# Performance work log

Measured on AMD Instinct MI355X. Metric: run time of the kernel, lower is better.

The kernel has to match this reference:

```python
import jax, jax.numpy as jnp
import numpy as np

N_NODES = 100000
N_EDGES = 1200000
D_IN = 64
D_HID = 64


def setup_inputs() -> dict:
    key = jax.random.key(0)
    ks = jax.random.split(key, 8)
    s = 1.0 / np.sqrt(D_IN)
    return {
        "x": jax.random.normal(ks[0], (N_NODES, D_IN), dtype=jnp.float32),
        "edge_index": jax.random.randint(ks[1], (2, N_EDGES), 0, N_NODES, dtype=jnp.int64),
        "W1_rel": jax.random.normal(ks[2], (D_IN, D_HID), dtype=jnp.float32) * s,
        "W1_root": jax.random.normal(ks[3], (D_IN, D_HID), dtype=jnp.float32) * s,
        "b1": jnp.zeros((D_HID,), dtype=jnp.float32),
        "W2_rel": jax.random.normal(ks[4], (D_HID, D_HID), dtype=jnp.float32) * s,
        "W2_root": jax.random.normal(ks[5], (D_HID, D_HID), dtype=jnp.float32) * s,
        "b2": jnp.zeros((D_HID,), dtype=jnp.float32),
        "Wc": jax.random.normal(ks[6], (D_HID, 2), dtype=jnp.float32) * s,
        "bc": jnp.zeros((2,), dtype=jnp.float32),
    }


def graph_conv(x, src, dst, W_rel, W_root, b):
    # sum_{j in N(i)} x_j  (scatter-add of src features onto dst), then linear
    aggr = jax.ops.segment_sum(x[src], dst, num_segments=x.shape[0])
    return aggr @ W_rel + x @ W_root + b


def reference(x, edge_index, W1_rel, W1_root, b1, W2_rel, W2_root, b2, Wc, bc):
    src, dst = edge_index[0], edge_index[1]
    h = jax.nn.relu(graph_conv(x, src, dst, W1_rel, W1_root, b1))
    h = jax.nn.relu(graph_conv(h, src, dst, W2_rel, W2_root, b2))
    return h.mean(axis=0) @ Wc + bc  # [2]
```

## Files before the change

### kernel.cpp

```cpp
#include <hip/hip_runtime.h>

#define D 64
#define ROWTILE 32
#define XPAD 68

__global__ void detect_kernel(const void* __restrict__ e, int* __restrict__ flag) {
    if (threadIdx.x == 0 && blockIdx.x == 0) {
        const int* p = (const int*)e;
        int is64 = 1;
        for (int i = 1; i < 64; i += 2) {
            if (p[i] != 0) { is64 = 0; break; }
        }
        *flag = is64;
    }
}

__device__ __forceinline__ void load_edge(const void* __restrict__ eidx, int is64,
                                          int e, int nE, int& src, int& dst) {
    if (is64) {
        const long long* p = (const long long*)eidx;
        src = (int)p[e];
        dst = (int)p[nE + e];
    } else {
        const int* p = (const int*)eidx;
        src = p[e];
        dst = p[nE + e];
    }
}

__global__ __launch_bounds__(256) void hist_kernel(
    const void* __restrict__ eidx, const int* __restrict__ flag,
    int* __restrict__ count, int nE)
{
    const int is64 = *flag;
    int e = blockIdx.x * 256 + threadIdx.x;
    if (e >= nE) return;
    int src, dst;
    load_edge(eidx, is64, e, nE, src, dst);
    atomicAdd(&count[dst], 1);
}

__global__ __launch_bounds__(256) void scan1_kernel(
    const int* __restrict__ count, int* __restrict__ offs,
    int* __restrict__ bsum, int N)
{
    __shared__ int tmp[256];
    const int tid = threadIdx.x;
    const int i = blockIdx.x * 256 + tid;
    int v = (i < N) ? count[i] : 0;
    tmp[tid] = v;
    __syncthreads();
#pragma unroll
    for (int off = 1; off < 256; off <<= 1) {
        int t = (tid >= off) ? tmp[tid - off] : 0;
        __syncthreads();
        tmp[tid] += t;
        __syncthreads();
    }
    int incl = tmp[tid];
    if (i < N) offs[i] = incl - v;
    if (tid == 255) bsum[blockIdx.x] = incl;
}

__global__ __launch_bounds__(1024) void scan2_kernel(int* __restrict__ bsum, int nblk)
{
    __shared__ int tmp[1024];
    const int tid = threadIdx.x;
    int v = (tid < nblk) ? bsum[tid] : 0;
    tmp[tid] = v;
    __syncthreads();
#pragma unroll
    for (int off = 1; off < 1024; off <<= 1) {
        int t = (tid >= off) ? tmp[tid - off] : 0;
        __syncthreads();
        tmp[tid] += t;
        __syncthreads();
    }
    if (tid < nblk) bsum[tid] = tmp[tid] - v;
}

__global__ __launch_bounds__(256) void scan3_kernel(
    int* __restrict__ offs, const int* __restrict__ bsum,
    int* __restrict__ cursor, int N, int E)
{
    const int i = blockIdx.x * 256 + threadIdx.x;
    if (i < N) {
        int v = offs[i] + bsum[blockIdx.x];
        offs[i] = v;
        cursor[i] = v;
    }
    if (i == 0) offs[N] = E;
}

__global__ __launch_bounds__(256) void scatterpos_kernel(
    const void* __restrict__ eidx, const int* __restrict__ flag,
    int* __restrict__ cursor, int* __restrict__ ssrc, int nE)
{
    const int is64 = *flag;
    int e = blockIdx.x * 256 + threadIdx.x;
    if (e >= nE) return;
    int src, dst;
    load_edge(eidx, is64, e, nE, src, dst);
    int pos = atomicAdd(&cursor[dst], 1);
    ssrc[pos] = src;
}

__global__ __launch_bounds__(256) void gather_aggr_kernel(
    const float* __restrict__ feat, const int* __restrict__ ssrc,
    const int* __restrict__ offs, float* __restrict__ aggr, int N)
{
    const int g = threadIdx.x >> 4;
    const int c = threadIdx.x & 15;
    const int n = blockIdx.x * 16 + g;
    if (n >= N) return;
    const int e0 = offs[n], e1 = offs[n + 1];
    float4 acc = make_float4(0.f, 0.f, 0.f, 0.f);
    for (int e = e0; e < e1; ++e) {
        int s = ssrc[e];
        float4 v = *(const float4*)(feat + (long long)s * D + c * 4);
        acc.x += v.x; acc.y += v.y; acc.z += v.z; acc.w += v.w;
    }
    *(float4*)(aggr + (long long)n * D + c * 4) = acc;
}

template <bool WRITE_OUT, bool WRITE_PART>
__global__ __launch_bounds__(256, 3) void linear_relu_kernel(
    const float* __restrict__ in, const float* __restrict__ aggr,
    const float* __restrict__ Wrel, const float* __restrict__ Wroot,
    const float* __restrict__ bias,
    float* __restrict__ out, float* __restrict__ acc_out, int N)
{
    __shared__ float xs[ROWTILE][XPAD];
    __shared__ float gs[ROWTILE][XPAD];
    __shared__ float pb[2][16][XPAD];
    __shared__ float red[4][D];

    const int tid  = threadIdx.x;
    const int lane = tid & 63;
    const int wid  = tid >> 6;
    const int pair = wid >> 1;
    const int role = wid & 1;

    float wv[D];
    {
        const float* W = role ? Wrel : Wroot;
#pragma unroll
        for (int k = 0; k < D; ++k) wv[k] = W[k * D + lane];
    }
    const float bv = bias[lane];

    float csum = 0.f;
    const int ntiles = (N + ROWTILE - 1) / ROWTILE;
    for (int tile = blockIdx.x; tile < ntiles; tile += gridDim.x) {
        const long long rowbase = (long long)tile * ROWTILE;
        __syncthreads();
#pragma unroll
        for (int it = 0; it < 2; ++it) {
            const int i = it * 256 + tid;
            const int r = i >> 4;
            const int c = i & 15;
            long long row = rowbase + r;
            if (row >= N) row = N - 1;
            const long long off = row * D + c * 4;
            *(float4*)&xs[r][c * 4] = *(const float4*)(in + off);
            *(float4*)&gs[r][c * 4] = *(const float4*)(aggr + off);
        }
        __syncthreads();
        float part[16];
#pragma unroll
        for (int g = 0; g < 4; ++g) {
            const int r0 = pair * 16 + g * 4;
            float a0 = 0.f, a1 = 0.f, a2 = 0.f, a3 = 0.f;
            const float (*src)[XPAD] = role ? gs : xs;
#pragma unroll
            for (int k4 = 0; k4 < D / 4; ++k4) {
                float4 f0 = *(const float4*)&src[r0 + 0][k4 * 4];
                float4 f1 = *(const float4*)&src[r0 + 1][k4 * 4];
                float4 f2 = *(const float4*)&src[r0 + 2][k4 * 4];
                float4 f3 = *(const float4*)&src[r0 + 3][k4 * 4];
                const float w0 = wv[4 * k4 + 0], w1 = wv[4 * k4 + 1];
                const float w2 = wv[4 * k4 + 2], w3 = wv[4 * k4 + 3];
                a0 = fmaf(f0.x, w0, a0); a0 = fmaf(f0.y, w1, a0);
                a0 = fmaf(f0.z, w2, a0); a0 = fmaf(f0.w, w3, a0);
                a1 = fmaf(f1.x, w0, a1); a1 = fmaf(f1.y, w1, a1);
                a1 = fmaf(f1.z, w2, a1); a1 = fmaf(f1.w, w3, a1);
                a2 = fmaf(f2.x, w0, a2); a2 = fmaf(f2.y, w1, a2);
                a2 = fmaf(f2.z, w2, a2); a2 = fmaf(f2.w, w3, a2);
                a3 = fmaf(f3.x, w0, a3); a3 = fmaf(f3.y, w1, a3);
                a3 = fmaf(f3.z, w2, a3); a3 = fmaf(f3.w, w3, a3);
            }
            part[g * 4 + 0] = a0; part[g * 4 + 1] = a1;
            part[g * 4 + 2] = a2; part[g * 4 + 3] = a3;
        }
        if (role == 1) {
#pragma unroll
            for (int r = 0; r < 16; ++r) pb[pair][r][lane] = part[r];
        }
        __syncthreads();
        if (role == 0) {
#pragma unroll
            for (int r = 0; r < 16; ++r) {
                const long long grow = rowbase + pair * 16 + r;
                const float o = fmaxf(part[r] + pb[pair][r][lane] + bv, 0.f);
                if (grow < N) {
                    if (WRITE_OUT) out[grow * D + lane] = o;
                    if (WRITE_PART) csum += o;
                }
            }
        }
    }

    if (WRITE_PART) {
        __syncthreads();
        red[wid][lane] = csum;
        __syncthreads();
        if (tid < D) {
            float s = red[0][tid] + red[1][tid] + red[2][tid] + red[3][tid];
            unsafeAtomicAdd(&acc_out[tid], s);
        }
    }
}

__global__ void final_kernel(const float* __restrict__ acc,
                             const float* __restrict__ Wc, const float* __restrict__ bc,
                             float* __restrict__ out, float invN)
{
    const int lane = threadIdx.x;
    float m  = acc[lane] * invN;
    float o0 = m * Wc[lane * 2 + 0];
    float o1 = m * Wc[lane * 2 + 1];
#pragma unroll
    for (int off = 32; off > 0; off >>= 1) {
        o0 += __shfl_down(o0, off);
        o1 += __shfl_down(o1, off);
    }
    if (lane == 0) {
        out[0] = o0 + bc[0];
        out[1] = o1 + bc[1];
    }
}

extern "C" void kernel_launch(void* const* d_in, const int* in_sizes, int n_in,
                              void* d_out, int out_size, void* d_ws, size_t ws_size,
                              hipStream_t stream)
{
    const float* x       = (const float*)d_in[0];
    const void*  eidx    = d_in[1];
    const float* W1_rel  = (const float*)d_in[2];
    const float* W1_root = (const float*)d_in[3];
    const float* b1      = (const float*)d_in[4];
    const float* W2_rel  = (const float*)d_in[5];
    const float* W2_root = (const float*)d_in[6];
    const float* b2      = (const float*)d_in[7];
    const float* Wc      = (const float*)d_in[8];
    const float* bc      = (const float*)d_in[9];
    float* out = (float*)d_out;

    const int N = in_sizes[0] / D;
    const int E = in_sizes[1] / 2;

    auto align256 = [](size_t v) { return (v + 255) & ~(size_t)255; };

    char* p = (char*)d_ws;
    const size_t featBytes = align256((size_t)N * D * sizeof(float));
    float* aggr   = (float*)p; p += featBytes;
    float* h1     = (float*)p; p += featBytes;
    float* acc    = (float*)p; p += align256((size_t)D * sizeof(float));
    int*   count  = (int*)p;   p += align256((size_t)N * sizeof(int));
    int*   cursor = (int*)p;   p += align256((size_t)N * sizeof(int));
    int*   offs   = (int*)p;   p += align256(((size_t)N + 1) * sizeof(int));
    int*   bsum   = (int*)p;   p += align256((size_t)1024 * sizeof(int));
    int*   ssrc   = (int*)p;   p += align256((size_t)E * sizeof(int));
    int*   flag   = (int*)p;

    const int eblocks = (E + 255) / 256;
    const int nblk    = (N + 255) / 256;

    detect_kernel<<<1, 64, 0, stream>>>(eidx, flag);
    hipMemsetAsync(count, 0, (size_t)N * sizeof(int), stream);
    hipMemsetAsync(acc, 0, (size_t)D * sizeof(float), stream);
    hist_kernel<<<eblocks, 256, 0, stream>>>(eidx, flag, count, E);
    scan1_kernel<<<nblk, 256, 0, stream>>>(count, offs, bsum, N);
    scan2_kernel<<<1, 1024, 0, stream>>>(bsum, nblk);
    scan3_kernel<<<nblk, 256, 0, stream>>>(offs, bsum, cursor, N, E);
    scatterpos_kernel<<<eblocks, 256, 0, stream>>>(eidx, flag, cursor, ssrc, E);

    const int ablocks = (N + 15) / 16;

    gather_aggr_kernel<<<ablocks, 256, 0, stream>>>(x, ssrc, offs, aggr, N);
    linear_relu_kernel<true, false><<<1024, 256, 0, stream>>>(
        x, aggr, W1_rel, W1_root, b1, h1, nullptr, N);

    gather_aggr_kernel<<<ablocks, 256, 0, stream>>>(h1, ssrc, offs, aggr, N);
    linear_relu_kernel<false, true><<<1024, 256, 0, stream>>>(
        h1, aggr, W2_rel, W2_root, b2, nullptr, acc, N);

    final_kernel<<<1, 64, 0, stream>>>(acc, Wc, bc, out, 1.0f / (float)N);
}
```

Before: 438.5 us.

## Replace per-edge global atomic CSR scatter with two-level bucketed scatter

Replaces the per-edge global atomicAdd cursor scatter with two passes. The first sorts each 4096-edge chunk in shared memory into 256-node buckets and writes them with one global atomic per bucket. The second builds the CSR per bucket using LDS atomics. The goal is to remove heavy global atomic contention and scattered writes across 100k cursors, at the cost of an extra 8-byte-per-edge intermediate buffer and an extra kernel. It also unrolls the gather loop.

New measurement: 362.2 us. -17.4%, faster.

```diff
diff --git a/kernel.cpp b/kernel.cpp
--- a/kernel.cpp
+++ b/kernel.cpp
@@ -3,6 +3,8 @@
 #define D 64
 #define ROWTILE 32
 #define XPAD 68
+#define CHUNK 4096
+#define NBMAX 512
 
 __global__ void detect_kernel(const void* __restrict__ e, int* __restrict__ flag) {
     if (threadIdx.x == 0 && blockIdx.x == 0) {
@@ -80,29 +82,102 @@
 }
 
 __global__ __launch_bounds__(256) void scan3_kernel(
-    int* __restrict__ offs, const int* __restrict__ bsum,
-    int* __restrict__ cursor, int N, int E)
+    int* __restrict__ offs, const int* __restrict__ bsum, int N, int E)
 {
     const int i = blockIdx.x * 256 + threadIdx.x;
-    if (i < N) {
-        int v = offs[i] + bsum[blockIdx.x];
-        offs[i] = v;
-        cursor[i] = v;
-    }
+    if (i < N) offs[i] += bsum[blockIdx.x];
     if (i == 0) offs[N] = E;
 }
 
-__global__ __launch_bounds__(256) void scatterpos_kernel(
+__global__ __launch_bounds__(256) void bucket_scatter_kernel(
     const void* __restrict__ eidx, const int* __restrict__ flag,
-    int* __restrict__ cursor, int* __restrict__ ssrc, int nE)
-{
+    const int* __restrict__ offs, int* __restrict__ gbcur,
+    uint2* __restrict__ ebuk, int nE, int N, int nbk)
+{
+    __shared__ int bcnt[NBMAX];
+    __shared__ int boffs[NBMAX];
+    __shared__ int brun[NBMAX];
+    __shared__ int gbase[NBMAX];
+    __shared__ int bstart[NBMAX];
+    __shared__ int ps[256];
+    __shared__ uint2 staged[CHUNK];
+
     const int is64 = *flag;
-    int e = blockIdx.x * 256 + threadIdx.x;
-    if (e >= nE) return;
-    int src, dst;
-    load_edge(eidx, is64, e, nE, src, dst);
-    int pos = atomicAdd(&cursor[dst], 1);
-    ssrc[pos] = src;
+    const int tid = threadIdx.x;
+    const int e0 = blockIdx.x * CHUNK;
+    const int ec = min(CHUNK, nE - e0);
+
+    for (int i = tid; i < NBMAX; i += 256) { bcnt[i] = 0; brun[i] = 0; }
+    for (int i = tid; i < nbk; i += 256) bstart[i] = offs[i << 8];
+    __syncthreads();
+
+#pragma unroll
+    for (int j = 0; j < CHUNK / 256; ++j) {
+        const int i = j * 256 + tid;
+        if (i < ec) {
+            int s, d;
+            load_edge(eidx, is64, e0 + i, nE, s, d);
+            atomicAdd(&bcnt[d >> 8], 1);
+        }
+    }
+    __syncthreads();
+
+    const int c0 = bcnt[2 * tid], c1 = bcnt[2 * tid + 1];
+    ps[tid] = c0 + c1;
+    __syncthreads();
+#pragma unroll
+    for (int off = 1; off < 256; off <<= 1) {
+        int t = (tid >= off) ? ps[tid - off] : 0;
+        __syncthreads();
+        ps[tid] += t;
+        __syncthreads();
+    }
+    const int pexcl = ps[tid] - (c0 + c1);
+    boffs[2 * tid]     = pexcl;
+    boffs[2 * tid + 1] = pexcl + c0;
+    if (c0 > 0) gbase[2 * tid]     = atomicAdd(&gbcur[2 * tid], c0);
+    if (c1 > 0) gbase[2 * tid + 1] = atomicAdd(&gbcur[2 * tid + 1], c1);
+    __syncthreads();
+
+#pragma unroll
+    for (int j = 0; j < CHUNK / 256; ++j) {
+        const int i = j * 256 + tid;
+        if (i < ec) {
+            int s, d;
+            load_edge(eidx, is64, e0 + i, nE, s, d);
+            const int b = d >> 8;
+            const int p = boffs[b] + atomicAdd(&brun[b], 1);
+            staged[p] = make_uint2((unsigned)s, (unsigned)d);
+        }
+    }
+    __syncthreads();
+
+    for (int i = tid; i < ec; i += 256) {
+        const uint2 ent = staged[i];
+        const int b = (int)(ent.y >> 8);
+        const int pos = bstart[b] + gbase[b] + (i - boffs[b]);
+        ebuk[pos] = ent;
+    }
+}
+
+__global__ __launch_bounds__(256) void bucket_csr_kernel(
+    const uint2* __restrict__ ebuk, const int* __restrict__ offs,
+    int* __restrict__ ssrc, int N)
+{
+    __shared__ int lcur[256];
+    const int b  = blockIdx.x;
+    const int n0 = b << 8;
+    const int nn = min(256, N - n0);
+    const int tid = threadIdx.x;
+    const int bs = offs[n0];
+    const int be = offs[min(n0 + 256, N)];
+    if (tid < nn) lcur[tid] = offs[n0 + tid];
+    __syncthreads();
+    for (int i = bs + tid; i < be; i += 256) {
+        const uint2 ent = ebuk[i];
+        const int pos = atomicAdd(&lcur[(int)ent.y - n0], 1);
+        ssrc[pos] = (int)ent.x;
+    }
 }
 
 __global__ __launch_bounds__(256) void gather_aggr_kernel(
@@ -115,6 +190,7 @@
     if (n >= N) return;
     const int e0 = offs[n], e1 = offs[n + 1];
     float4 acc = make_float4(0.f, 0.f, 0.f, 0.f);
+#pragma unroll 4
     for (int e = e0; e < e1; ++e) {
         int s = ssrc[e];
         float4 v = *(const float4*)(feat + (long long)s * D + c * 4);
@@ -267,23 +343,29 @@
     float* h1     = (float*)p; p += featBytes;
     float* acc    = (float*)p; p += align256((size_t)D * sizeof(float));
     int*   count  = (int*)p;   p += align256((size_t)N * sizeof(int));
-    int*   cursor = (int*)p;   p += align256((size_t)N * sizeof(int));
     int*   offs   = (int*)p;   p += align256(((size_t)N + 1) * sizeof(int));
     int*   bsum   = (int*)p;   p += align256((size_t)1024 * sizeof(int));
+    int*   gbcur  = (int*)p;   p += align256((size_t)NBMAX * sizeof(int));
     int*   ssrc   = (int*)p;   p += align256((size_t)E * sizeof(int));
+    uint2* ebuk   = (uint2*)p; p += align256((size_t)E * sizeof(uint2));
     int*   flag   = (int*)p;
 
     const int eblocks = (E + 255) / 256;
     const int nblk    = (N + 255) / 256;
+    const int nbk     = (N + 255) >> 8;
+    const int cblocks = (E + CHUNK - 1) / CHUNK;
 
     detect_kernel<<<1, 64, 0, stream>>>(eidx, flag);
     hipMemsetAsync(count, 0, (size_t)N * sizeof(int), stream);
     hipMemsetAsync(acc, 0, (size_t)D * sizeof(float), stream);
+    hipMemsetAsync(gbcur, 0, (size_t)NBMAX * sizeof(int), stream);
     hist_kernel<<<eblocks, 256, 0, stream>>>(eidx, flag, count, E);
     scan1_kernel<<<nblk, 256, 0, stream>>>(count, offs, bsum, N);
     scan2_kernel<<<1, 1024, 0, stream>>>(bsum, nblk);
-    scan3_kernel<<<nblk, 256, 0, stream>>>(offs, bsum, cursor, N, E);
-    scatterpos_kernel<<<eblocks, 256, 0, stream>>>(eidx, flag, cursor, ssrc, E);
+    scan3_kernel<<<nblk, 256, 0, stream>>>(offs, bsum, N, E);
+    bucket_scatter_kernel<<<cblocks, 256, 0, stream>>>(
+        eidx, flag, offs, gbcur, ebuk, E, N, nbk);
+    bucket_csr_kernel<<<nbk, 256, 0, stream>>>(ebuk, offs, ssrc, N);
 
     const int ablocks = (N + 15) / 16;
 
```
